# Performance work log

Measured on AMD Instinct MI355X. Metric: run time of the kernel, lower is better.

Reference implementation:

```python
import jax, jax.numpy as jnp
import numpy as np

N_E = 8192
E_DIM = 256
BETA = 0.25


def setup_inputs() -> dict:
    key = jax.random.key(0)
    k1, k2 = jax.random.split(key)
    z = jax.random.normal(k1, (16, 1024, E_DIM), dtype=jnp.float32)
    # matches embedding.weight.data.uniform_(-1/n_e, 1/n_e)
    embedding = jax.random.uniform(k2, (N_E, E_DIM), dtype=jnp.float32,
                                   minval=-1.0 / N_E, maxval=1.0 / N_E)
    return {"z": z, "embedding": embedding}


def reference(z, embedding):
    B, S, D = z.shape  # [16, 1024, 256]
    zf = z.reshape(-1, D)  # [N, D], N = B*S
    # squared L2 distances to every codebook entry: [N, n_e]
    d = (jnp.sum(zf * zf, axis=1, keepdims=True)
         + jnp.sum(embedding * embedding, axis=1)
         - 2.0 * (zf @ embedding.T))
    min_encoding_indices = jnp.argmin(d, axis=1)  # [N]
    # one-hot encodings (returned by the module) [N, n_e]
    min_encodings = jax.nn.one_hot(min_encoding_indices, N_E, dtype=jnp.float32)
    # z_q = min_encodings @ embedding == gather of nearest codes
    z_q = embedding[min_encoding_indices].reshape(z.shape)  # [B, S, D]
    sg = jax.lax.stop_gradient
    loss = jnp.mean((sg(z_q) - z) ** 2) + BETA * jnp.mean((z_q - sg(z)) ** 2)
    # straight-through estimator
    z_q_st = z + sg(z_q - z)
    e_mean = jnp.mean(min_encodings, axis=0)  # [n_e]
    perplexity = jnp.exp(-jnp.sum(e_mean * jnp.log(e_mean + 1e-10)))
    return (loss, z_q_st, perplexity, min_encodings, min_encoding_indices[:, None])
```

## Files before the change

kernel.cpp:

```cpp
#include <hip/hip_runtime.h>
#include <cstddef>

#define NROWS 16384
#define NE    8192
#define DD    256

typedef unsigned long long u64;
typedef float vf4 __attribute__((ext_vector_type(4)));
typedef short bf16x8 __attribute__((ext_vector_type(8)));
typedef float f32x4 __attribute__((ext_vector_type(4)));
typedef unsigned short us8 __attribute__((ext_vector_type(8)));

#define OH_TOT ((size_t)NROWS * NE)
#define OH_VEC ((OH_TOT - 4) / 4)
#define CAND_CAP 4000000
#define LLIST_CAP 2048

__global__ __launch_bounds__(256) void k_rowsq(
    const float* __restrict__ z, const float* __restrict__ emb,
    float* __restrict__ zsq, float* __restrict__ esq,
    u64* __restrict__ best, int* __restrict__ counts,
    float* __restrict__ wadd, int* __restrict__ cand_n)
{
  const int g = blockIdx.x * 256 + threadIdx.x;
  if (g == 0) *cand_n = 0;
  if (g < NE) counts[g] = 0;
  if (g < NROWS) best[g] = ~0ull;

  const float* row;
  float* outp;
  if (g < NROWS) { row = z + (size_t)g * DD;            outp = zsq + g; }
  else           { row = emb + (size_t)(g - NROWS) * DD; outp = esq + (g - NROWS); }

  float sa = 0.0f;
  float half_s[2];
#pragma unroll
  for (int h = 0; h < 2; ++h) {
    const float* p = row + h * 128;
    float r[8];
    {
      const float4 v0 = *(const float4*)(p);
      const float4 v1 = *(const float4*)(p + 4);
      const float xs[8] = {v0.x, v0.y, v0.z, v0.w, v1.x, v1.y, v1.z, v1.w};
#pragma unroll
      for (int j = 0; j < 8; ++j) {
        float sq = xs[j] * xs[j];
        asm volatile("" : "+v"(sq));
        r[j] = sq;
        sa += fabsf(xs[j]);
      }
    }
    for (int i = 8; i < 128; i += 8) {
      const float4 v0 = *(const float4*)(p + i);
      const float4 v1 = *(const float4*)(p + i + 4);
      const float xs[8] = {v0.x, v0.y, v0.z, v0.w, v1.x, v1.y, v1.z, v1.w};
#pragma unroll
      for (int j = 0; j < 8; ++j) {
        float sq = xs[j] * xs[j];
        asm volatile("" : "+v"(sq));
        r[j] = r[j] + sq;
        sa += fabsf(xs[j]);
      }
    }
    half_s[h] = ((r[0] + r[1]) + (r[2] + r[3])) + ((r[4] + r[5]) + (r[6] + r[7]));
  }
  const float zs = half_s[0] + half_s[1];
  *outp = zs;
  if (g < NROWS)
    wadd[g] = 2.0f * ((zs + 2.0f) * 1.2e-7f + 2.0f * (1.0e-6f * sa) + 5.0e-8f);
}

__device__ __forceinline__ unsigned short f2bf_rne(float f) {
  const unsigned u = __float_as_uint(f);
  return (unsigned short)((u + 0x7FFFu + ((u >> 16) & 1u)) >> 16);
}
__device__ __forceinline__ unsigned encf(float f) {
  const unsigned u = __float_as_uint(f);
  return (u & 0x80000000u) ? ~u : (u | 0x80000000u);
}
__device__ __forceinline__ float decf(unsigned k) {
  const unsigned u = (k & 0x80000000u) ? (k ^ 0x80000000u) : ~k;
  return __uint_as_float(u);
}

__global__ __launch_bounds__(512, 2) void k_screen(
    const float* __restrict__ z, const float* __restrict__ emb,
    const float* __restrict__ esq, const float* __restrict__ wadd,
    unsigned* __restrict__ cand, int* __restrict__ cand_n,
    float* __restrict__ ohbase)
{
  __shared__ unsigned short Bs[2][128][256];
  __shared__ unsigned smin[128];
  __shared__ float wl[128];
  __shared__ unsigned llist[LLIST_CAP];
  __shared__ unsigned lcnt;
  __shared__ unsigned gbase;

  const int tid = threadIdx.x;
  const int b = blockIdx.x;
  const int x = b & 7, q = b >> 3;
  const int half = x & 1;
  const int panel = q * 4 + (x >> 1);
  const int R0 = panel * 128;
  const int C0 = half * 4096;

  const int wave = tid >> 6;
  const int lane = tid & 63;
  const int l15 = lane & 15;
  const int kg = lane >> 4;
  const int wr = (wave >> 2) * 64;
  const int wc = (wave & 3) * 32;
  const int cb0 = wc + l15;
  const int cb1 = cb0 + 16;

  const int c_st = tid >> 2;
  const int kq = tid & 3;
  const int swz = c_st & 7;

  if (tid < 128) { smin[tid] = 0xFFFFFFFFu; wl[tid] = wadd[R0 + tid]; }
  if (tid == 0) lcnt = 0;

  float* zp0 = ohbase + 2;
  size_t zt = (size_t)b * 131072 + tid;
  const vf4 zzero = {0.0f, 0.0f, 0.0f, 0.0f};
  if (b == 0 && tid == 0) { ohbase[0] = 0.0f; ohbase[1] = 0.0f; }
  if (b == 255 && tid == 0) { ohbase[OH_TOT - 2] = 0.0f; ohbase[OH_TOT - 1] = 0.0f; }

  bf16x8 af[4][8];
#pragma unroll
  for (int i = 0; i < 4; ++i) {
    const float* zp_ = z + (size_t)(R0 + wr + i * 16 + l15) * DD + kg * 8;
#pragma unroll
    for (int kt = 0; kt < 8; ++kt) {
      const float4 a0 = *(const float4*)(zp_ + kt * 32);
      const float4 a1 = *(const float4*)(zp_ + kt * 32 + 4);
      bf16x8 w;
      w[0] = (short)f2bf_rne(a0.x); w[1] = (short)f2bf_rne(a0.y);
      w[2] = (short)f2bf_rne(a0.z); w[3] = (short)f2bf_rne(a0.w);
      w[4] = (short)f2bf_rne(a1.x); w[5] = (short)f2bf_rne(a1.y);
      w[6] = (short)f2bf_rne(a1.z); w[7] = (short)f2bf_rne(a1.w);
      af[i][kt] = w;
    }
  }

  float runmin[16];
#pragma unroll
  for (int i = 0; i < 16; ++i) runmin[i] = 1e30f;

#define SSTAGE(BUF_, TT_)                                                   \
  {                                                                         \
    const float* ep = emb + (size_t)(C0 + (TT_) * 128 + c_st) * DD + kq * 64;\
    unsigned short* dst = &Bs[BUF_][c_st][0];                               \
    _Pragma("unroll")                                                       \
    for (int s = 0; s < 4; ++s) {                                           \
      const float4 f0 = *(const float4*)(ep + 16 * s);                      \
      const float4 f1 = *(const float4*)(ep + 16 * s + 4);                  \
      const float4 f2 = *(const float4*)(ep + 16 * s + 8);                  \
      const float4 f3 = *(const float4*)(ep + 16 * s + 12);                 \
      us8 u0, u1;                                                           \
      u0[0] = f2bf_rne(f0.x); u0[1] = f2bf_rne(f0.y);                       \
      u0[2] = f2bf_rne(f0.z); u0[3] = f2bf_rne(f0.w);                       \
      u0[4] = f2bf_rne(f1.x); u0[5] = f2bf_rne(f1.y);                       \
      u0[6] = f2bf_rne(f1.z); u0[7] = f2bf_rne(f1.w);                       \
      u1[0] = f2bf_rne(f2.x); u1[1] = f2bf_rne(f2.y);                       \
      u1[2] = f2bf_rne(f2.z); u1[3] = f2bf_rne(f2.w);                       \
      u1[4] = f2bf_rne(f3.x); u1[5] = f2bf_rne(f3.y);                       \
      u1[6] = f2bf_rne(f3.z); u1[7] = f2bf_rne(f3.w);                       \
      const int ch0 = (kq * 8 + 2 * s) ^ swz;                               \
      const int ch1 = (kq * 8 + 2 * s + 1) ^ swz;                           \
      *(us8*)(dst + ch0 * 8) = u0;                                          \
      *(us8*)(dst + ch1 * 8) = u1;                                          \
    }                                                                       \
  }

#define PUSH(E_)                                                            \
  {                                                                         \
    const unsigned s_ = atomicAdd(&lcnt, 1u);                               \
    if (s_ < LLIST_CAP) llist[s_] = (E_);                                   \
    else { const int g_ = atomicAdd(cand_n, 1);                             \
           if (g_ < CAND_CAP) cand[g_] = (E_); }                            \
  }

  SSTAGE(0, 0);
  __syncthreads();

  for (int t = 0; t < 32; ++t) {
    const int Cb = C0 + t * 128;
    if (t + 1 < 32) SSTAGE((t + 1) & 1, t + 1);

#pragma unroll
    for (int s = 0; s < 8; ++s) {
      if (zt < OH_VEC) __builtin_nontemporal_store(zzero, (vf4*)(zp0 + 4 * zt));
      zt += 512;
    }

    f32x4 acc[4][2];
#pragma unroll
    for (int i = 0; i < 4; ++i) {
      acc[i][0] = (f32x4){0.0f, 0.0f, 0.0f, 0.0f};
      acc[i][1] = (f32x4){0.0f, 0.0f, 0.0f, 0.0f};
    }
    {
      const int bbuf = t & 1;
#pragma unroll
      for (int kt = 0; kt < 8; ++kt) {
        const bf16x8 b0 = *(const bf16x8*)(&Bs[bbuf][cb0][0] + (((kt * 4 + kg) ^ (cb0 & 7)) * 8));
        const bf16x8 b1 = *(const bf16x8*)(&Bs[bbuf][cb1][0] + (((kt * 4 + kg) ^ (cb1 & 7)) * 8));
#pragma unroll
        for (int i = 0; i < 4; ++i) {
          acc[i][0] = __builtin_amdgcn_mfma_f32_16x16x32_bf16(af[i][kt], b0, acc[i][0], 0, 0, 0);
          acc[i][1] = __builtin_amdgcn_mfma_f32_16x16x32_bf16(af[i][kt], b1, acc[i][1], 0, 0, 0);
        }
      }
    }

    const float ev0 = esq[Cb + cb0];
    const float ev1 = esq[Cb + cb1];

#pragma unroll
    for (int i = 0; i < 4; ++i)
#pragma unroll
      for (int r = 0; r < 4; ++r) {
        const float rv0 = ev0 - 2.0f * acc[i][0][r];
        const float rv1 = ev1 - 2.0f * acc[i][1][r];
        runmin[i * 4 + r] = fminf(runmin[i * 4 + r], fminf(rv0, rv1));
      }

    if (t < 4 || (t & 3) == 3) {
#pragma unroll
      for (int i = 0; i < 4; ++i)
#pragma unroll
        for (int r = 0; r < 4; ++r) {
          float mn = runmin[i * 4 + r];
          mn = fminf(mn, __shfl_xor(mn, 1, 16));
          mn = fminf(mn, __shfl_xor(mn, 2, 16));
          mn = fminf(mn, __shfl_xor(mn, 4, 16));
          mn = fminf(mn, __shfl_xor(mn, 8, 16));
          if (l15 == 0) atomicMin(&smin[wr + i * 16 + kg * 4 + r], encf(mn));
        }
    }
    __syncthreads();

#pragma unroll
    for (int i = 0; i < 4; ++i)
#pragma unroll
      for (int r = 0; r < 4; ++r) {
        const int Rl = wr + i * 16 + kg * 4 + r;
        const float thrf = decf(smin[Rl]) + wl[Rl];
        const float rv0 = ev0 - 2.0f * acc[i][0][r];
        const float rv1 = ev1 - 2.0f * acc[i][1][r];
        if (rv0 <= thrf) PUSH(((unsigned)(R0 + Rl) << 13) | (unsigned)(Cb + cb0));
        if (rv1 <= thrf) PUSH(((unsigned)(R0 + Rl) << 13) | (unsigned)(Cb + cb1));
      }
  }

  __syncthreads();
  const unsigned n = (lcnt < LLIST_CAP) ? lcnt : LLIST_CAP;
  if (tid == 0) gbase = (unsigned)atomicAdd(cand_n, (int)n);
  __syncthreads();
  for (unsigned idx = tid; idx < n; idx += 512) {
    const unsigned g = gbase + idx;
    if (g < CAND_CAP) cand[g] = llist[idx];
  }
}

__global__ __launch_bounds__(256) void k_recheck(
    const float* __restrict__ z, const float* __restrict__ emb,
    const float* __restrict__ zsq, const float* __restrict__ esq,
    const unsigned* __restrict__ cand, const int* __restrict__ cand_n,
    u64* __restrict__ best)
{
  const int n = min(*cand_n, CAND_CAP);
  for (int i = blockIdx.x * 256 + threadIdx.x; i < n; i += gridDim.x * 256) {
    const unsigned e = cand[i];
    const int row = (int)(e >> 13);
    const int col = (int)(e & (NE - 1));
    const float4* zr = (const float4*)(z + (size_t)row * DD);
    const float4* er = (const float4*)(emb + (size_t)col * DD);
    float dot = 0.0f;
#pragma unroll 8
    for (int q = 0; q < 64; ++q) {
      const float4 a = zr[q];
      const float4 b = er[q];
      dot = fmaf(a.x, b.x, dot);
      dot = fmaf(a.y, b.y, dot);
      dot = fmaf(a.z, b.z, dot);
      dot = fmaf(a.w, b.w, dot);
    }
    const float s1 = zsq[row] + esq[col];
    const float dv = s1 - 2.0f * dot;
    atomicMin(&best[row], ((u64)__float_as_uint(dv) << 32) | (unsigned)col);
  }
}

__global__ __launch_bounds__(256) void k_gather2(
    const float* __restrict__ z, const float* __restrict__ emb,
    const u64* __restrict__ best,
    float* __restrict__ out_zq, float* __restrict__ out_onehot,
    float* __restrict__ out_idx, float* __restrict__ partials,
    int* __restrict__ counts)
{
  __shared__ float sred[256];
  const int row = blockIdx.x * 4 + (threadIdx.x >> 6);
  const int lane = threadIdx.x & 63;
  const int idx = (int)(unsigned)(best[row] & 0xffffffffull);
  const int k0 = lane * 4;

  const float4 e  = *(const float4*)(emb + (size_t)idx * DD + k0);
  const float4 zv = *(const float4*)(z + (size_t)row * DD + k0);
  *(float4*)(out_zq + (size_t)row * DD + k0) = e;

  const float dx = e.x - zv.x, dy = e.y - zv.y, dz = e.z - zv.z, dw = e.w - zv.w;
  sred[threadIdx.x] = dx * dx + dy * dy + dz * dz + dw * dw;

  if (lane == 0) {
    out_idx[row] = (float)idx;
    out_onehot[(size_t)row * NE + idx] = 1.0f;
    atomicAdd(&counts[idx], 1);
  }
  __syncthreads();
  for (int s = 128; s > 0; s >>= 1) {
    if (threadIdx.x < s) sred[threadIdx.x] += sred[threadIdx.x + s];
    __syncthreads();
  }
  if (threadIdx.x == 0) partials[blockIdx.x] = sred[0];
}

__global__ __launch_bounds__(256) void k_final(
    const int* __restrict__ counts, const float* __restrict__ partials,
    float* __restrict__ out_loss, float* __restrict__ out_perp)
{
  __shared__ float sred[256];
  __shared__ float sl[256];
  float le = 0.0f;
  for (int e = threadIdx.x; e < NE; e += 256) {
    const float p = (float)counts[e] * (1.0f / 16384.0f);
    le += p * logf(p + 1e-10f);
  }
  float ll = 0.0f;
  for (int b = threadIdx.x; b < NROWS / 4; b += 256) ll += partials[b];
  sred[threadIdx.x] = le;
  sl[threadIdx.x] = ll;
  __syncthreads();
  for (int s = 128; s > 0; s >>= 1) {
    if (threadIdx.x < s) {
      sred[threadIdx.x] += sred[threadIdx.x + s];
      sl[threadIdx.x] += sl[threadIdx.x + s];
    }
    __syncthreads();
  }
  if (threadIdx.x == 0) {
    *out_perp = expf(-sred[0]);
    *out_loss = sl[0] * (1.25f / 4194304.0f);
  }
}

extern "C" void kernel_launch(void* const* d_in, const int* in_sizes, int n_in,
                              void* d_out, int out_size, void* d_ws, size_t ws_size,
                              hipStream_t stream) {
  const float* z   = (const float*)d_in[0];
  const float* emb = (const float*)d_in[1];

  float* out        = (float*)d_out;
  float* out_loss   = out;
  float* out_zq     = out + 1;
  float* out_perp   = out + 4194305;
  float* out_onehot = out + 4194306;
  float* out_idx    = out + 138412034;

  float* zsq      = (float*)d_ws;
  float* esq      = zsq + NROWS;
  u64*   best     = (u64*)(esq + NE);
  int*   counts   = (int*)(best + NROWS);
  float* partials = (float*)(counts + NE);
  float* wadd     = partials + 4096;
  int*   cand_n   = (int*)(wadd + NROWS);

  unsigned* cand = (unsigned*)out_zq;

  k_rowsq<<<96, 256, 0, stream>>>(z, emb, zsq, esq, best, counts, wadd, cand_n);
  k_screen<<<256, 512, 0, stream>>>(z, emb, esq, wadd, cand, cand_n, out_onehot);
  k_recheck<<<512, 256, 0, stream>>>(z, emb, zsq, esq, cand, cand_n, best);
  k_gather2<<<NROWS / 4, 256, 0, stream>>>(z, emb, best, out_zq, out_onehot,
                                           out_idx, partials, counts);
  k_final<<<1, 256, 0, stream>>>(counts, partials, out_loss, out_perp);
}
```

Baseline: 908.4 us.

## Pre-convert codebook to bf16 and screen from global memory with smaller tiles

The codebook is converted to bf16 once in the row-norm kernel, so the screening kernel no longer converts fp32 codes per tile. Shared-memory staging of B is dropped: each wave reads bf16 code vectors straight from global/L2 into MFMA. Tiles shrink to 64 rows by 2048 codes over 1024 blocks of 256 threads. Thresholds now live in per-thread registers that are refreshed periodically, and early steps are replayed at the end. This trades LDS reuse for more L2 traffic and a little workspace, and the candidate buffer moves into the workspace.

```diff
diff --git a/kernel.cpp b/kernel.cpp
--- a/kernel.cpp
+++ b/kernel.cpp
@@ -20,7 +20,8 @@
     const float* __restrict__ z, const float* __restrict__ emb,
     float* __restrict__ zsq, float* __restrict__ esq,
     u64* __restrict__ best, int* __restrict__ counts,
-    float* __restrict__ wadd, int* __restrict__ cand_n)
+    float* __restrict__ wadd, int* __restrict__ cand_n,
+    unsigned short* __restrict__ eb)
 {
   const int g = blockIdx.x * 256 + threadIdx.x;
   if (g == 0) *cand_n = 0;
@@ -66,8 +67,24 @@
   }
   const float zs = half_s[0] + half_s[1];
   *outp = zs;
-  if (g < NROWS)
+  if (g < NROWS) {
     wadd[g] = 2.0f * ((zs + 2.0f) * 1.2e-7f + 2.0f * (1.0e-6f * sa) + 5.0e-8f);
+  } else {
+    unsigned short* er = eb + (size_t)(g - NROWS) * DD;
+#pragma unroll 4
+    for (int c = 0; c < DD; c += 8) {
+      const float4 v0 = *(const float4*)(row + c);
+      const float4 v1 = *(const float4*)(row + c + 4);
+      us8 u;
+      const float xs[8] = {v0.x, v0.y, v0.z, v0.w, v1.x, v1.y, v1.z, v1.w};
+#pragma unroll
+      for (int j = 0; j < 8; ++j) {
+        const unsigned b = __float_as_uint(xs[j]);
+        u[j] = (unsigned short)((b + 0x7FFFu + ((b >> 16) & 1u)) >> 16);
+      }
+      *(us8*)(er + c) = u;
+    }
+  }
 }
 
 __device__ __forceinline__ unsigned short f2bf_rne(float f) {
@@ -83,53 +100,43 @@
   return __uint_as_float(u);
 }
 
-__global__ __launch_bounds__(512, 2) void k_screen(
-    const float* __restrict__ z, const float* __restrict__ emb,
+__global__ __launch_bounds__(256) void k_screen(
+    const float* __restrict__ z, const unsigned short* __restrict__ eb,
     const float* __restrict__ esq, const float* __restrict__ wadd,
     unsigned* __restrict__ cand, int* __restrict__ cand_n,
     float* __restrict__ ohbase)
 {
-  __shared__ unsigned short Bs[2][128][256];
-  __shared__ unsigned smin[128];
-  __shared__ float wl[128];
+  __shared__ unsigned smin[64];
+  __shared__ float wl[64];
   __shared__ unsigned llist[LLIST_CAP];
   __shared__ unsigned lcnt;
   __shared__ unsigned gbase;
 
   const int tid = threadIdx.x;
   const int b = blockIdx.x;
-  const int x = b & 7, q = b >> 3;
-  const int half = x & 1;
-  const int panel = q * 4 + (x >> 1);
-  const int R0 = panel * 128;
-  const int C0 = half * 4096;
+  const int x = b & 7;
+  const int quarter = x >> 1;
+  const int panel = (b >> 3) * 2 + (x & 1);
+  const int R0 = panel * 64;
+  const int C0 = quarter * 2048;
 
   const int wave = tid >> 6;
   const int lane = tid & 63;
   const int l15 = lane & 15;
   const int kg = lane >> 4;
-  const int wr = (wave >> 2) * 64;
-  const int wc = (wave & 3) * 32;
-  const int cb0 = wc + l15;
-  const int cb1 = cb0 + 16;
-
-  const int c_st = tid >> 2;
-  const int kq = tid & 3;
-  const int swz = c_st & 7;
-
-  if (tid < 128) { smin[tid] = 0xFFFFFFFFu; wl[tid] = wadd[R0 + tid]; }
+
+  if (tid < 64) { smin[tid] = 0xFFFFFFFFu; wl[tid] = wadd[R0 + tid]; }
   if (tid == 0) lcnt = 0;
 
   float* zp0 = ohbase + 2;
-  size_t zt = (size_t)b * 131072 + tid;
+  size_t zt = (size_t)b * 32768 + tid;
   const vf4 zzero = {0.0f, 0.0f, 0.0f, 0.0f};
   if (b == 0 && tid == 0) { ohbase[0] = 0.0f; ohbase[1] = 0.0f; }
-  if (b == 255 && tid == 0) { ohbase[OH_TOT - 2] = 0.0f; ohbase[OH_TOT - 1] = 0.0f; }
-
-  bf16x8 af[4][8];
-#pragma unroll
-  for (int i = 0; i < 4; ++i) {
-    const float* zp_ = z + (size_t)(R0 + wr + i * 16 + l15) * DD + kg * 8;
+  if (b == 1023 && tid == 0) { ohbase[OH_TOT - 2] = 0.0f; ohbase[OH_TOT - 1] = 0.0f; }
+
+  bf16x8 af[8];
+  {
+    const float* zp_ = z + (size_t)(R0 + wave * 16 + l15) * DD + kg * 8;
 #pragma unroll
     for (int kt = 0; kt < 8; ++kt) {
       const float4 a0 = *(const float4*)(zp_ + kt * 32);
@@ -139,39 +146,15 @@
       w[2] = (short)f2bf_rne(a0.z); w[3] = (short)f2bf_rne(a0.w);
       w[4] = (short)f2bf_rne(a1.x); w[5] = (short)f2bf_rne(a1.y);
       w[6] = (short)f2bf_rne(a1.z); w[7] = (short)f2bf_rne(a1.w);
-      af[i][kt] = w;
-    }
-  }
-
-  float runmin[16];
-#pragma unroll
-  for (int i = 0; i < 16; ++i) runmin[i] = 1e30f;
-
-#define SSTAGE(BUF_, TT_)                                                   \
-  {                                                                         \
-    const float* ep = emb + (size_t)(C0 + (TT_) * 128 + c_st) * DD + kq * 64;\
-    unsigned short* dst = &Bs[BUF_][c_st][0];                               \
-    _Pragma("unroll")                                                       \
-    for (int s = 0; s < 4; ++s) {                                           \
-      const float4 f0 = *(const float4*)(ep + 16 * s);                      \
-      const float4 f1 = *(const float4*)(ep + 16 * s + 4);                  \
-      const float4 f2 = *(const float4*)(ep + 16 * s + 8);                  \
-      const float4 f3 = *(const float4*)(ep + 16 * s + 12);                 \
-      us8 u0, u1;                                                           \
-      u0[0] = f2bf_rne(f0.x); u0[1] = f2bf_rne(f0.y);                       \
-      u0[2] = f2bf_rne(f0.z); u0[3] = f2bf_rne(f0.w);                       \
-      u0[4] = f2bf_rne(f1.x); u0[5] = f2bf_rne(f1.y);                       \
-      u0[6] = f2bf_rne(f1.z); u0[7] = f2bf_rne(f1.w);                       \
-      u1[0] = f2bf_rne(f2.x); u1[1] = f2bf_rne(f2.y);                       \
-      u1[2] = f2bf_rne(f2.z); u1[3] = f2bf_rne(f2.w);                       \
-      u1[4] = f2bf_rne(f3.x); u1[5] = f2bf_rne(f3.y);                       \
-      u1[6] = f2bf_rne(f3.z); u1[7] = f2bf_rne(f3.w);                       \
-      const int ch0 = (kq * 8 + 2 * s) ^ swz;                               \
-      const int ch1 = (kq * 8 + 2 * s + 1) ^ swz;                           \
-      *(us8*)(dst + ch0 * 8) = u0;                                          \
-      *(us8*)(dst + ch1 * 8) = u1;                                          \
-    }                                                                       \
-  }
+      af[kt] = w;
+    }
+  }
+  __syncthreads();
+
+  const int rbase = wave * 16 + kg * 4;
+  float wlr[4], thr[4], rm[4];
+#pragma unroll
+  for (int r = 0; r < 4; ++r) { wlr[r] = wl[rbase + r]; thr[r] = 1e30f; rm[r] = 1e30f; }
 
 #define PUSH(E_)                                                            \
   {                                                                         \
@@ -181,86 +164,79 @@
            if (g_ < CAND_CAP) cand[g_] = (E_); }                            \
   }
 
-  SSTAGE(0, 0);
-  __syncthreads();
-
-  for (int t = 0; t < 32; ++t) {
-    const int Cb = C0 + t * 128;
-    if (t + 1 < 32) SSTAGE((t + 1) & 1, t + 1);
-
-#pragma unroll
-    for (int s = 0; s < 8; ++s) {
-      if (zt < OH_VEC) __builtin_nontemporal_store(zzero, (vf4*)(zp0 + 4 * zt));
-      zt += 512;
-    }
-
-    f32x4 acc[4][2];
-#pragma unroll
-    for (int i = 0; i < 4; ++i) {
-      acc[i][0] = (f32x4){0.0f, 0.0f, 0.0f, 0.0f};
-      acc[i][1] = (f32x4){0.0f, 0.0f, 0.0f, 0.0f};
-    }
-    {
-      const int bbuf = t & 1;
-#pragma unroll
-      for (int kt = 0; kt < 8; ++kt) {
-        const bf16x8 b0 = *(const bf16x8*)(&Bs[bbuf][cb0][0] + (((kt * 4 + kg) ^ (cb0 & 7)) * 8));
-        const bf16x8 b1 = *(const bf16x8*)(&Bs[bbuf][cb1][0] + (((kt * 4 + kg) ^ (cb1 & 7)) * 8));
-#pragma unroll
-        for (int i = 0; i < 4; ++i) {
-          acc[i][0] = __builtin_amdgcn_mfma_f32_16x16x32_bf16(af[i][kt], b0, acc[i][0], 0, 0, 0);
-          acc[i][1] = __builtin_amdgcn_mfma_f32_16x16x32_bf16(af[i][kt], b1, acc[i][1], 0, 0, 0);
-        }
-      }
-    }
-
-    const float ev0 = esq[Cb + cb0];
-    const float ev1 = esq[Cb + cb1];
-
-#pragma unroll
-    for (int i = 0; i < 4; ++i)
-#pragma unroll
-      for (int r = 0; r < 4; ++r) {
-        const float rv0 = ev0 - 2.0f * acc[i][0][r];
-        const float rv1 = ev1 - 2.0f * acc[i][1][r];
-        runmin[i * 4 + r] = fminf(runmin[i * 4 + r], fminf(rv0, rv1));
-      }
-
-    if (t < 4 || (t & 3) == 3) {
-#pragma unroll
-      for (int i = 0; i < 4; ++i)
-#pragma unroll
-        for (int r = 0; r < 4; ++r) {
-          float mn = runmin[i * 4 + r];
-          mn = fminf(mn, __shfl_xor(mn, 1, 16));
-          mn = fminf(mn, __shfl_xor(mn, 2, 16));
-          mn = fminf(mn, __shfl_xor(mn, 4, 16));
-          mn = fminf(mn, __shfl_xor(mn, 8, 16));
-          if (l15 == 0) atomicMin(&smin[wr + i * 16 + kg * 4 + r], encf(mn));
-        }
-    }
-    __syncthreads();
-
-#pragma unroll
-    for (int i = 0; i < 4; ++i)
-#pragma unroll
-      for (int r = 0; r < 4; ++r) {
-        const int Rl = wr + i * 16 + kg * 4 + r;
-        const float thrf = decf(smin[Rl]) + wl[Rl];
-        const float rv0 = ev0 - 2.0f * acc[i][0][r];
-        const float rv1 = ev1 - 2.0f * acc[i][1][r];
-        if (rv0 <= thrf) PUSH(((unsigned)(R0 + Rl) << 13) | (unsigned)(Cb + cb0));
-        if (rv1 <= thrf) PUSH(((unsigned)(R0 + Rl) << 13) | (unsigned)(Cb + cb1));
-      }
-  }
+#define STEPBODY(S_, EMIT_, DOZ_)                                           \
+  {                                                                         \
+    const int c0 = C0 + (S_) * 32 + l15;                                    \
+    const int c1 = c0 + 16;                                                 \
+    const bf16x8* bp0 = (const bf16x8*)(eb + (size_t)c0 * DD) + kg;         \
+    const bf16x8* bp1 = (const bf16x8*)(eb + (size_t)c1 * DD) + kg;         \
+    f32x4 a0 = (f32x4){0.0f, 0.0f, 0.0f, 0.0f};                             \
+    f32x4 a1 = (f32x4){0.0f, 0.0f, 0.0f, 0.0f};                             \
+    _Pragma("unroll")                                                       \
+    for (int kt = 0; kt < 8; ++kt) {                                        \
+      a0 = __builtin_amdgcn_mfma_f32_16x16x32_bf16(af[kt], bp0[kt * 4], a0, 0, 0, 0); \
+      a1 = __builtin_amdgcn_mfma_f32_16x16x32_bf16(af[kt], bp1[kt * 4], a1, 0, 0, 0); \
+    }                                                                       \
+    if (DOZ_) {                                                             \
+      if (zt < OH_VEC) __builtin_nontemporal_store(zzero, (vf4*)(zp0 + 4 * zt)); \
+      zt += 256;                                                            \
+      if (zt < OH_VEC) __builtin_nontemporal_store(zzero, (vf4*)(zp0 + 4 * zt)); \
+      zt += 256;                                                            \
+    }                                                                       \
+    const float ev0 = esq[c0];                                              \
+    const float ev1 = esq[c1];                                              \
+    float rv0[4], rv1[4];                                                   \
+    float gm = 1e30f;                                                       \
+    _Pragma("unroll")                                                       \
+    for (int r = 0; r < 4; ++r) {                                           \
+      rv0[r] = ev0 - 2.0f * a0[r];                                          \
+      rv1[r] = ev1 - 2.0f * a1[r];                                          \
+      const float mn = fminf(rv0[r], rv1[r]);                               \
+      rm[r] = fminf(rm[r], mn);                                             \
+      gm = fminf(gm, mn - thr[r]);                                          \
+    }                                                                       \
+    if ((EMIT_) && gm <= 0.0f) {                                            \
+      _Pragma("unroll")                                                     \
+      for (int r = 0; r < 4; ++r) {                                         \
+        if (rv0[r] <= thr[r]) PUSH(((unsigned)(R0 + rbase + r) << 13) | (unsigned)c0); \
+        if (rv1[r] <= thr[r]) PUSH(((unsigned)(R0 + rbase + r) << 13) | (unsigned)c1); \
+      }                                                                     \
+    }                                                                       \
+  }
+
+#define FLUSH_REFRESH                                                       \
+  {                                                                         \
+    _Pragma("unroll")                                                       \
+    for (int r = 0; r < 4; ++r) {                                           \
+      float mn = rm[r];                                                     \
+      mn = fminf(mn, __shfl_xor(mn, 1, 16));                                \
+      mn = fminf(mn, __shfl_xor(mn, 2, 16));                                \
+      mn = fminf(mn, __shfl_xor(mn, 4, 16));                                \
+      mn = fminf(mn, __shfl_xor(mn, 8, 16));                                \
+      if (l15 == 0) atomicMin(&smin[rbase + r], encf(mn));                  \
+    }                                                                       \
+    _Pragma("unroll")                                                       \
+    for (int r = 0; r < 4; ++r) thr[r] = decf(smin[rbase + r]) + wlr[r];    \
+  }
+
+  for (int s = 0; s < 64; ++s) {
+    STEPBODY(s, (s >= 2), 1);
+    if (s == 1 || (s & 7) == 7) FLUSH_REFRESH;
+  }
+
+  __syncthreads();
+#pragma unroll
+  for (int r = 0; r < 4; ++r) thr[r] = decf(smin[rbase + r]) + wlr[r];
+  STEPBODY(0, 1, 0);
+  STEPBODY(1, 1, 0);
 
   __syncthreads();
   const unsigned n = (lcnt < LLIST_CAP) ? lcnt : LLIST_CAP;
   if (tid == 0) gbase = (unsigned)atomicAdd(cand_n, (int)n);
   __syncthreads();
-  for (unsigned idx = tid; idx < n; idx += 512) {
-    const unsigned g = gbase + idx;
-    if (g < CAND_CAP) cand[g] = llist[idx];
+  for (unsigned i = tid; i < n; i += 256) {
+    const unsigned g = gbase + i;
+    if (g < CAND_CAP) cand[g] = llist[i];
   }
 }
 
@@ -375,11 +351,11 @@
   float* partials = (float*)(counts + NE);
   float* wadd     = partials + 4096;
   int*   cand_n   = (int*)(wadd + NROWS);
-
-  unsigned* cand = (unsigned*)out_zq;
-
-  k_rowsq<<<96, 256, 0, stream>>>(z, emb, zsq, esq, best, counts, wadd, cand_n);
-  k_screen<<<256, 512, 0, stream>>>(z, emb, esq, wadd, cand, cand_n, out_onehot);
+  unsigned short* eb = (unsigned short*)(wadd + NROWS + 4);
+  unsigned* cand  = (unsigned*)(eb + (size_t)NE * DD);
+
+  k_rowsq<<<96, 256, 0, stream>>>(z, emb, zsq, esq, best, counts, wadd, cand_n, eb);
+  k_screen<<<1024, 256, 0, stream>>>(z, eb, esq, wadd, cand, cand_n, out_onehot);
   k_recheck<<<512, 256, 0, stream>>>(z, emb, zsq, esq, cand, cand_n, best);
   k_gather2<<<NROWS / 4, 256, 0, stream>>>(z, emb, best, out_zq, out_onehot,
                                            out_idx, partials, counts);
```

Measured after the change: 1.243 ms. +36.9%, slower.
